# Optimization experiments

Hardware: AMD Instinct MI355X
Metric: run time of the kernel (lower is better)

The kernel has to match this reference:

```python
import jax, jax.numpy as jnp
import numpy as np

N, D_IN, H, M = 16384, 360, 512, 2048


def _linear(x, W, b):
    return x @ W.T + b


def _bidir_softmax(Q, K):
    # score[i, j] = <Q_i, K_j>
    s = Q @ K.T                      # [N, M]
    return jax.nn.softmax(s, axis=0), jax.nn.softmax(s, axis=1)


def _read(Q, K):
    sq, sm = _bidir_softmax(Q, K)
    upd = Q * (jax.lax.stop_gradient(sm) @ K)   # elementwise gate by attended memory
    return upd, sq, sm


def _un_read(Q, K):
    # scores computed against -K, but memory combine still uses K (as in torch source)
    sq, sm = _bidir_softmax(Q, -K)
    upd = Q * (jax.lax.stop_gradient(sm) @ K)
    return upd, sq, sm


def _upload(Q, K):
    sq, sm = _bidir_softmax(Q, K)
    m, d = K.shape
    g = jnp.argmax(sm, axis=1)                       # top-1 slot per query  [N]
    col_max = jnp.max(sq, axis=0)                    # max over queries per slot [m]
    n = Q.shape[0]
    w = sq[jnp.arange(n), g] / col_max[g]            # per-query weight [N]
    # vectorized form of the per-slot python loop: scatter-reduce weighted queries
    query_update = jax.ops.segment_sum(w[:, None] * Q, g, num_segments=m)  # [m, d]
    upd = query_update + K
    norm = jnp.linalg.norm(upd, axis=1, keepdims=True)
    upd = upd / jnp.maximum(norm, 1e-12)             # F.normalize(dim=1)
    return jax.lax.stop_gradient(upd)


def setup_inputs() -> dict:
    key = jax.random.key(0)
    ks = jax.random.split(key, 12)
    s = 0.02
    return {
        "x": jax.random.normal(ks[0], (N, D_IN), jnp.float32),
        "m_items_1": jax.random.normal(ks[1], (M, H), jnp.float32),
        "W1": jax.random.normal(ks[2], (H, D_IN), jnp.float32) * s,
        "b1": jnp.zeros((H,), jnp.float32),
        "W2": jax.random.normal(ks[3], (H, H), jnp.float32) * s,
        "b2": jnp.zeros((H,), jnp.float32),
        "W3": jax.random.normal(ks[4], (H, H), jnp.float32) * s,
        "b3": jnp.zeros((H,), jnp.float32),
        "Wd": jax.random.normal(ks[5], (1, H), jnp.float32) * s,
        "bd": jnp.zeros((1,), jnp.float32),
        "train": 1,
    }


def reference(x, m_items_1, W1, b1, W2, b2, W3, b3, Wd, bd, train):
    h = jax.nn.relu(_linear(x, W1, b1))
    h = jax.nn.relu(_linear(h, W2, b2))   # dropout=0.0 -> identity
    h = jax.nn.relu(_linear(h, W3, b3))
    pred_min_p, _, _ = _read(h, m_items_1)
    pred_min_n, _, _ = _un_read(h, m_items_1)
    mem = _upload(h, m_items_1) if train else m_items_1
    pred = _linear(h, Wd, bd)
    return (pred, pred_min_n, pred_min_p, mem)
```

## Files before the change

kernel.cpp:

```cpp
#include <hip/hip_runtime.h>
#include <math.h>

#define N_ROWS 16384
#define D_INN  360
#define KP1    384
#define HID    512
#define M_SLOTS 2048

typedef __attribute__((ext_vector_type(8))) short short8v;
typedef __attribute__((ext_vector_type(4))) float f32x4;
typedef __attribute__((address_space(1))) unsigned int as1_uint;
typedef __attribute__((address_space(3))) unsigned int as3_uint;

__device__ __forceinline__ unsigned short bf16_rne(float f){
  unsigned u = __float_as_uint(f);
  unsigned r = u + 0x7FFFu + ((u >> 16) & 1u);
  return (unsigned short)(r >> 16);
}
__device__ __forceinline__ float bf16_to_f32(unsigned short h){
  return __uint_as_float(((unsigned)h) << 16);
}

__device__ __forceinline__ unsigned fmap(float f){
  unsigned u = __float_as_uint(f);
  return (u & 0x80000000u) ? ~u : (u | 0x80000000u);
}
__device__ __forceinline__ float funmap(unsigned u){
  unsigned b = (u & 0x80000000u) ? (u ^ 0x80000000u) : ~u;
  return __uint_as_float(b);
}

__device__ __forceinline__ void glds16(const void* g, void* l){
  __builtin_amdgcn_global_load_lds((const as1_uint*)g, (as3_uint*)l, 16, 0, 0);
}

__device__ __forceinline__ float4 ld4bf(const unsigned short* hi, const unsigned short* lo, size_t off){
  uint2 h = *(const uint2*)(hi + off);
  uint2 l = *(const uint2*)(lo + off);
  float4 r;
  r.x = bf16_to_f32((unsigned short)(h.x & 0xffffu)) + bf16_to_f32((unsigned short)(l.x & 0xffffu));
  r.y = bf16_to_f32((unsigned short)(h.x >> 16))     + bf16_to_f32((unsigned short)(l.x >> 16));
  r.z = bf16_to_f32((unsigned short)(h.y & 0xffffu)) + bf16_to_f32((unsigned short)(l.y & 0xffffu));
  r.w = bf16_to_f32((unsigned short)(h.y >> 16))     + bf16_to_f32((unsigned short)(l.y >> 16));
  return r;
}


__device__ __forceinline__ void split_body(const float* __restrict__ src,
                                           unsigned short* __restrict__ hi,
                                           unsigned short* __restrict__ lo, int b){
  int idx = (b*256 + (int)threadIdx.x) * 8;
  float4 a = *(const float4*)&src[idx];
  float4 bb = *(const float4*)&src[idx+4];
  float v[8] = {a.x,a.y,a.z,a.w,bb.x,bb.y,bb.z,bb.w};
  short8v hv, lv;
#pragma unroll
  for (int e=0;e<8;++e){
    unsigned short h = bf16_rne(v[e]);
    hv[e] = (short)h;
    lv[e] = (short)bf16_rne(v[e] - bf16_to_f32(h));
  }
  *(short8v*)&hi[idx] = hv;
  *(short8v*)&lo[idx] = lv;
}

__device__ __forceinline__ void pad_split_body(const float* __restrict__ src,
                                               unsigned short* __restrict__ hi,
                                               unsigned short* __restrict__ lo,
                                               int R, int Ksrc, int Kp, int b){
  long long e0 = ((long long)b*256 + threadIdx.x) * 4;
  if (e0 >= (long long)R*Kp) return;
  int row = (int)(e0 / Kp), c = (int)(e0 % Kp);
  unsigned short h4[4], l4[4];
  if (c < Ksrc){
    float4 v = *(const float4*)&src[(size_t)row*Ksrc + c];
    float vv[4] = {v.x, v.y, v.z, v.w};
#pragma unroll
    for (int e=0;e<4;++e){
      unsigned short h = bf16_rne(vv[e]);
      h4[e] = h;
      l4[e] = bf16_rne(vv[e] - bf16_to_f32(h));
    }
  } else {
#pragma unroll
    for (int e=0;e<4;++e){ h4[e]=0; l4[e]=0; }
  }
  *(uint2*)&hi[(size_t)row*Kp + c] = *(uint2*)h4;
  *(uint2*)&lo[(size_t)row*Kp + c] = *(uint2*)l4;
}

__global__ __launch_bounds__(256) void init_all(
    const float* __restrict__ x,  const float* __restrict__ W1,
    const float* __restrict__ W2, const float* __restrict__ W3,
    const float* __restrict__ Km,
    unsigned short* __restrict__ xph,  unsigned short* __restrict__ xpl,
    unsigned short* __restrict__ W1ph, unsigned short* __restrict__ W1pl,
    unsigned short* __restrict__ W2h,  unsigned short* __restrict__ W2l,
    unsigned short* __restrict__ W3h,  unsigned short* __restrict__ W3l,
    unsigned short* __restrict__ Khi,  unsigned short* __restrict__ Klo,
    unsigned short* __restrict__ Kt,
    float* __restrict__ qacc, int* __restrict__ cnt,
    unsigned* __restrict__ colmaxU)
{
  __shared__ float tile[64][65];
  int b = blockIdx.x;
  const int t = threadIdx.x;
  if (b < 6144){ pad_split_body(x, xph, xpl, N_ROWS, D_INN, KP1, b); return; }
  b -= 6144;
  if (b < 192){ pad_split_body(W1, W1ph, W1pl, HID, D_INN, KP1, b); return; }
  b -= 192;
  if (b < 128){ split_body(W2, W2h, W2l, b); return; }
  b -= 128;
  if (b < 128){ split_body(W3, W3h, W3l, b); return; }
  b -= 128;
  if (b < 512){ split_body(Km, Khi, Klo, b); return; }
  b -= 512;
  if (b < 256){
    const int sb = (b & 31) * 64;
    const int hb = (b >> 5) * 64;
    {
      int r = t >> 2, cq = t & 3;
#pragma unroll
      for (int q=0;q<4;++q){
        float4 v = *(const float4*)&Km[(size_t)(sb+r)*HID + hb + cq*16 + q*4];
        tile[r][cq*16+q*4+0]=v.x; tile[r][cq*16+q*4+1]=v.y;
        tile[r][cq*16+q*4+2]=v.z; tile[r][cq*16+q*4+3]=v.w;
      }
    }
    __syncthreads();
    {
      int hl = t >> 2, sq = t & 3;
      unsigned short w16[16];
#pragma unroll
      for (int q=0;q<16;++q) w16[q] = bf16_rne(tile[sq*16+q][hl]);
      *(uint4*)&Kt[(size_t)(hb+hl)*M_SLOTS + sb + sq*16]     = *(uint4*)&w16[0];
      *(uint4*)&Kt[(size_t)(hb+hl)*M_SLOTS + sb + sq*16 + 8] = *(uint4*)&w16[8];
    }
    return;
  }
  b -= 256;
  if (b < 512){
    int idx = (b*256 + t)*8;
    float4 z = {0.f,0.f,0.f,0.f};
    *(float4*)&qacc[idx]     = z;
    *(float4*)&qacc[idx + 4] = z;
    return;
  }
  b -= 512;
  { int i = b*256 + t; if (i < M_SLOTS){ cnt[i] = 0; colmaxU[i] = 0u; } }
}

__global__ __launch_bounds__(512) void mlp_gemm(
    const unsigned short* __restrict__ Ah_g, const unsigned short* __restrict__ Al_g,
    const unsigned short* __restrict__ Wh_g, const unsigned short* __restrict__ Wl_g,
    const float* __restrict__ bias,
    unsigned short* __restrict__ Ohi, unsigned short* __restrict__ Olo,
    int Kp, const float* __restrict__ Wd, float* __restrict__ ppart)
{
  __shared__ char smem[65536];
  unsigned short* Ah = (unsigned short*)smem;
  unsigned short* Al = (unsigned short*)(smem + 16384);
  unsigned short* Bh = (unsigned short*)(smem + 32768);
  unsigned short* Bl = (unsigned short*)(smem + 49152);
  const int t = threadIdx.x;
  const int lane = t & 63, w = t >> 6;
  const int l15 = lane & 15, l4 = lane >> 4;
  const int rowBase = blockIdx.x * 128;
  const int colBase = blockIdx.y * 128;
  const int wr = (w >> 1) * 32;
  const int wc = (w & 1) * 64;

  f32x4 acc[2][4];
#pragma unroll
  for (int i=0;i<2;++i)
#pragma unroll
    for (int j=0;j<4;++j) acc[i][j] = (f32x4){0.f,0.f,0.f,0.f};

  const int nkt = Kp >> 6;
  for (int kt = 0; kt < nkt; ++kt){
    const int k0 = kt * 64;
#pragma unroll
    for (int p = 0; p < 2; ++p){
      int idx = p*512 + t;
      int r = idx >> 3, c = idx & 7;
      int cc = c ^ (r & 7);
      size_t go = (size_t)(rowBase + r) * Kp + (k0 + cc*8);
      glds16(Ah_g + go, (char*)Ah + idx*16);
      glds16(Al_g + go, (char*)Al + idx*16);
    }
#pragma unroll
    for (int p = 0; p < 2; ++p){
      int idx = p*512 + t;
      int r = idx >> 3, c = idx & 7;
      int cc = c ^ (r & 7);
      size_t go = (size_t)(colBase + r) * Kp + (k0 + cc*8);
      glds16(Wh_g + go, (char*)Bh + idx*16);
      glds16(Wl_g + go, (char*)Bl + idx*16);
    }
    __syncthreads();

#pragma unroll
    for (int s = 0; s < 2; ++s){
      short8v a_h[2], a_l[2], b_h[4], b_l[4];
#pragma unroll
      for (int rt = 0; rt < 2; ++rt){
        int r = wr + rt*16 + l15;
        int off = r*128 + ((s*4 + l4) ^ (r & 7))*16;
        a_h[rt] = *(const short8v*)((const char*)Ah + off);
        a_l[rt] = *(const short8v*)((const char*)Al + off);
      }
#pragma unroll
      for (int ct = 0; ct < 4; ++ct){
        int r = wc + ct*16 + l15;
        int off = r*128 + ((s*4 + l4) ^ (r & 7))*16;
        b_h[ct] = *(const short8v*)((const char*)Bh + off);
        b_l[ct] = *(const short8v*)((const char*)Bl + off);
      }
#pragma unroll
      for (int rt = 0; rt < 2; ++rt)
#pragma unroll
        for (int ct = 0; ct < 4; ++ct){
          acc[rt][ct] = __builtin_amdgcn_mfma_f32_16x16x32_bf16(a_h[rt], b_h[ct], acc[rt][ct], 0,0,0);
          acc[rt][ct] = __builtin_amdgcn_mfma_f32_16x16x32_bf16(a_h[rt], b_l[ct], acc[rt][ct], 0,0,0);
          acc[rt][ct] = __builtin_amdgcn_mfma_f32_16x16x32_bf16(a_l[rt], b_h[ct], acc[rt][ct], 0,0,0);
        }
    }
    __syncthreads();
  }

  float bcol[4];
#pragma unroll
  for (int ct=0; ct<4; ++ct) bcol[ct] = bias[colBase + wc + ct*16 + l15];
  unsigned short* Sout = (unsigned short*)smem;
#pragma unroll
  for (int rt=0; rt<2; ++rt)
#pragma unroll
    for (int ct=0; ct<4; ++ct)
#pragma unroll
      for (int reg=0; reg<4; ++reg){
        float v = acc[rt][ct][reg] + bcol[ct];
        v = v > 0.f ? v : 0.f;
        acc[rt][ct][reg] = v;
        Sout[(wr + rt*16 + l4*4 + reg)*136 + wc + ct*16 + l15] = bf16_rne(v);
      }

  if (ppart){
    float wdv[4];
#pragma unroll
    for (int ct=0; ct<4; ++ct) wdv[ct] = Wd[colBase + wc + ct*16 + l15];
#pragma unroll
    for (int rt=0; rt<2; ++rt)
#pragma unroll
      for (int reg=0; reg<4; ++reg){
        float pd = acc[rt][0][reg]*wdv[0] + acc[rt][1][reg]*wdv[1]
                 + acc[rt][2][reg]*wdv[2] + acc[rt][3][reg]*wdv[3];
#pragma unroll
        for (int d=1; d<16; d<<=1) pd += __shfl_xor(pd, d);
        if (l15 == 0){
          int row = rowBase + wr + rt*16 + l4*4 + reg;
          ppart[(size_t)row*8 + (colBase >> 7)*2 + (wc >> 6)] = pd;
        }
      }
  }

  __syncthreads();
#pragma unroll
  for (int p = 0; p < 4; ++p){
    int row = (t >> 4) + p*32;
    int c8 = (t & 15) * 8;
    uint4 v = *(uint4*)&Sout[row*136 + c8];
    *(uint4*)&Ohi[(size_t)(rowBase+row)*HID + colBase + c8] = v;
  }
  __syncthreads();
#pragma unroll
  for (int rt=0; rt<2; ++rt)
#pragma unroll
    for (int ct=0; ct<4; ++ct)
#pragma unroll
      for (int reg=0; reg<4; ++reg){
        float v = acc[rt][ct][reg];
        unsigned short h = bf16_rne(v);
        Sout[(wr + rt*16 + l4*4 + reg)*136 + wc + ct*16 + l15] = bf16_rne(v - bf16_to_f32(h));
      }
  __syncthreads();
#pragma unroll
  for (int p = 0; p < 4; ++p){
    int row = (t >> 4) + p*32;
    int c8 = (t & 15) * 8;
    uint4 v = *(uint4*)&Sout[row*136 + c8];
    *(uint4*)&Olo[(size_t)(rowBase+row)*HID + colBase + c8] = v;
  }
}

__global__ __launch_bounds__(512) void sgemm_stats(
    const unsigned short* __restrict__ Qhi, const unsigned short* __restrict__ Qlo,
    const unsigned short* __restrict__ Khi, const unsigned short* __restrict__ Klo,
    unsigned short* __restrict__ Sb,
    float* __restrict__ pmax, int* __restrict__ pcol,
    float* __restrict__ psum, float* __restrict__ pnmax, float* __restrict__ pnsum,
    unsigned* __restrict__ colmaxU)
{
  __shared__ char smem[65536];
  unsigned short* Ah = (unsigned short*)smem;
  unsigned short* Al = (unsigned short*)(smem + 16384);
  unsigned short* Bh = (unsigned short*)(smem + 32768);
  unsigned short* Bl = (unsigned short*)(smem + 49152);
  const int t = threadIdx.x;
  const int lane = t & 63, w = t >> 6;
  const int l15 = lane & 15, l4 = lane >> 4;
  const int cb = blockIdx.x;
  const int rb = blockIdx.y;
  const int rowBase = rb * 128;
  const int colBase = cb * 128;
  const int wr = (w >> 1) * 32;
  const int wc = (w & 1) * 64;

  f32x4 acc[2][4];
#pragma unroll
  for (int i=0;i<2;++i)
#pragma unroll
    for (int j=0;j<4;++j) acc[i][j] = (f32x4){0.f,0.f,0.f,0.f};

  for (int kt = 0; kt < 8; ++kt){
    const int k0 = kt * 64;
#pragma unroll
    for (int p = 0; p < 2; ++p){
      int idx = p*512 + t;
      int r = idx >> 3, c = idx & 7;
      int cc = c ^ (r & 7);
      size_t go = (size_t)(rowBase + r) * HID + (k0 + cc*8);
      glds16(Qhi + go, (char*)Ah + idx*16);
      glds16(Qlo + go, (char*)Al + idx*16);
    }
#pragma unroll
    for (int p = 0; p < 2; ++p){
      int idx = p*512 + t;
      int r = idx >> 3, c = idx & 7;
      int cc = c ^ (r & 7);
      size_t go = (size_t)(colBase + r) * HID + (k0 + cc*8);
      glds16(Khi + go, (char*)Bh + idx*16);
      glds16(Klo + go, (char*)Bl + idx*16);
    }
    __syncthreads();

#pragma unroll
    for (int s = 0; s < 2; ++s){
      short8v a_h[2], a_l[2], b_h[4], b_l[4];
#pragma unroll
      for (int rt = 0; rt < 2; ++rt){
        int r = wr + rt*16 + l15;
        int off = r*128 + ((s*4 + l4) ^ (r & 7))*16;
        a_h[rt] = *(const short8v*)((const char*)Ah + off);
        a_l[rt] = *(const short8v*)((const char*)Al + off);
      }
#pragma unroll
      for (int ct = 0; ct < 4; ++ct){
        int r = wc + ct*16 + l15;
        int off = r*128 + ((s*4 + l4) ^ (r & 7))*16;
        b_h[ct] = *(const short8v*)((const char*)Bh + off);
        b_l[ct] = *(const short8v*)((const char*)Bl + off);
      }
#pragma unroll
      for (int rt = 0; rt < 2; ++rt)
#pragma unroll
        for (int ct = 0; ct < 4; ++ct){
          acc[rt][ct] = __builtin_amdgcn_mfma_f32_16x16x32_bf16(a_h[rt], b_h[ct], acc[rt][ct], 0,0,0);
          acc[rt][ct] = __builtin_amdgcn_mfma_f32_16x16x32_bf16(a_h[rt], b_l[ct], acc[rt][ct], 0,0,0);
          acc[rt][ct] = __builtin_amdgcn_mfma_f32_16x16x32_bf16(a_l[rt], b_h[ct], acc[rt][ct], 0,0,0);
        }
    }
    __syncthreads();
  }

#pragma unroll
  for (int rt = 0; rt < 2; ++rt){
#pragma unroll
    for (int reg = 0; reg < 4; ++reg){
      float v0 = acc[rt][0][reg], v1 = acc[rt][1][reg];
      float v2 = acc[rt][2][reg], v3 = acc[rt][3][reg];
      float bvv = v0; int bcc = colBase + wc + l15;
      if (v1 > bvv){ bvv = v1; bcc = colBase + wc + 16 + l15; }
      if (v2 > bvv){ bvv = v2; bcc = colBase + wc + 32 + l15; }
      if (v3 > bvv){ bvv = v3; bcc = colBase + wc + 48 + l15; }
      float mnv = fminf(fminf(v0,v1), fminf(v2,v3));
#pragma unroll
      for (int d = 1; d < 16; d <<= 1){
        float ov = __shfl_xor(bvv, d);
        int   oc = __shfl_xor(bcc, d);
        float om = __shfl_xor(mnv, d);
        if (ov > bvv || (ov == bvv && oc < bcc)){ bvv = ov; bcc = oc; }
        mnv = fminf(mnv, om);
      }
      float sp = __expf(v0-bvv)+__expf(v1-bvv)+__expf(v2-bvv)+__expf(v3-bvv);
      float sn = __expf(mnv-v0)+__expf(mnv-v1)+__expf(mnv-v2)+__expf(mnv-v3);
#pragma unroll
      for (int d = 1; d < 16; d <<= 1){ sp += __shfl_xor(sp,d); sn += __shfl_xor(sn,d); }
      if (l15 == 0){
        int row = rowBase + wr + rt*16 + l4*4 + reg;
        size_t pi = (size_t)row*32 + cb*2 + (w & 1);
        pmax[pi] = bvv; pcol[pi] = bcc; psum[pi] = sp;
        pnmax[pi] = -mnv; pnsum[pi] = sn;
      }
    }
  }

#pragma unroll
  for (int ct = 0; ct < 4; ++ct){
    float cm = -1e30f;
#pragma unroll
    for (int rt=0; rt<2; ++rt)
#pragma unroll
      for (int reg=0; reg<4; ++reg) cm = fmaxf(cm, acc[rt][ct][reg]);
    cm = fmaxf(cm, __shfl_xor(cm, 16));
    cm = fmaxf(cm, __shfl_xor(cm, 32));
    if (l4 == 0)
      atomicMax(&colmaxU[colBase + wc + ct*16 + l15], fmap(cm));
  }

  __syncthreads();
  unsigned short* Sout = (unsigned short*)smem;
#pragma unroll
  for (int rt=0; rt<2; ++rt)
#pragma unroll
    for (int ct=0; ct<4; ++ct)
#pragma unroll
      for (int reg=0; reg<4; ++reg)
        Sout[(wr + rt*16 + l4*4 + reg)*136 + wc + ct*16 + l15] = bf16_rne(acc[rt][ct][reg]);
  __syncthreads();
#pragma unroll
  for (int p = 0; p < 4; ++p){
    int row = (t >> 4) + p*32;
    int c8 = (t & 15) * 8;
    uint4 v = *(uint4*)&Sout[row*136 + c8];
    *(uint4*)&Sb[(size_t)(rowBase+row)*M_SLOTS + colBase + c8] = v;
  }
}

__global__ __launch_bounds__(256) void merge_all(
    const float* __restrict__ pmax, const int* __restrict__ pcol,
    const float* __restrict__ psum, const float* __restrict__ pnmax,
    const float* __restrict__ pnsum,
    float* __restrict__ rowm, float* __restrict__ rsp,
    float* __restrict__ rmn, float* __restrict__ rsn, int* __restrict__ gidx,
    int* __restrict__ cnt,
    const float* __restrict__ ppart, const float* __restrict__ bd,
    float* __restrict__ pred)
{
  int row = blockIdx.x*256 + threadIdx.x;
  const size_t base = (size_t)row*32;
  float m = -1e30f; int g = 0;
  for (int i=0;i<32;++i){
    float v = pmax[base+i];
    if (v > m){ m = v; g = pcol[base+i]; }
  }
  float s = 0.f;
  for (int i=0;i<32;++i) s += psum[base+i] * __expf(pmax[base+i]-m);
  float mn = -1e30f;
  for (int i=0;i<32;++i) mn = fmaxf(mn, pnmax[base+i]);
  float sn = 0.f;
  for (int i=0;i<32;++i) sn += pnsum[base+i] * __expf(pnmax[base+i]-mn);
  rowm[row]=m; gidx[row]=g; rsp[row]=1.f/s; rmn[row]=mn; rsn[row]=1.f/sn;
  atomicAdd(&cnt[g], 1);
  float pd = bd[0];
#pragma unroll
  for (int i=0;i<8;++i) pd += ppart[(size_t)row*8 + i];
  pred[row] = pd;
}

#define PV_RB 64
#define PV_HB 256
__global__ __launch_bounds__(512) void pv2(
    const unsigned short* __restrict__ Sb, const unsigned short* __restrict__ Kt,
    const float* __restrict__ rowm, const float* __restrict__ rsp,
    const float* __restrict__ rmn, const float* __restrict__ rsn,
    const unsigned short* __restrict__ Qhi, const unsigned short* __restrict__ Qlo,
    float* __restrict__ outP, float* __restrict__ outN)
{
  __shared__ char smem[49152];
  unsigned short* Ktile = (unsigned short*)smem;
  unsigned short* Wp = (unsigned short*)(smem + 32768);
  unsigned short* Wn = (unsigned short*)(smem + 40960);
  const int t = threadIdx.x, lane = t & 63, w = t >> 6;
  const int l15 = lane & 15, l4 = lane >> 4;
  const int rowBase = blockIdx.y * PV_RB;
  const int hBase = blockIdx.x * PV_HB;
  const int wrq = (w >> 2) * 32;
  const int hw = (w & 3) * 64;
  const int rS = t >> 3;
  const int c8 = t & 7;
  const float mp = rowm[rowBase + rS], mn = rmn[rowBase + rS];

  f32x4 accP[2][4], accN[2][4];
#pragma unroll
  for (int i=0;i<2;++i)
#pragma unroll
    for (int j=0;j<4;++j){ accP[i][j]=(f32x4){0.f,0.f,0.f,0.f}; accN[i][j]=(f32x4){0.f,0.f,0.f,0.f}; }

  for (int kt = 0; kt < 32; ++kt){
    const int k0 = kt*64;
#pragma unroll
    for (int p=0;p<4;++p){
      int idx = p*512 + t;
      int r = idx >> 3, c = idx & 7;
      int cc = c ^ (r & 7);
      glds16(Kt + (size_t)(hBase + r)*M_SLOTS + k0 + cc*8, (char*)Ktile + idx*16);
    }
    short8v sv = *(const short8v*)&Sb[(size_t)(rowBase + rS)*M_SLOTS + k0 + c8*8];
    short8v wp, wn;
#pragma unroll
    for (int e=0;e<8;++e){
      float sval = bf16_to_f32((unsigned short)sv[e]);
      wp[e] = (short)bf16_rne(__expf(sval - mp));
      wn[e] = (short)bf16_rne(__expf(-sval - mn));
    }
    {
      int ch = rS*8 + (c8 ^ (rS & 7));
      *(short8v*)(Wp + ch*8) = wp;
      *(short8v*)(Wn + ch*8) = wn;
    }
    __syncthreads();
#pragma unroll
    for (int s=0; s<2; ++s){
      short8v ap[2], an[2], b[4];
#pragma unroll
      for (int rt=0; rt<2; ++rt){
        int r = wrq + rt*16 + l15;
        int ch = r*8 + ((s*4 + l4) ^ (r & 7));
        ap[rt] = *(const short8v*)(Wp + ch*8);
        an[rt] = *(const short8v*)(Wn + ch*8);
      }
#pragma unroll
      for (int ct=0; ct<4; ++ct){
        int hr = hw + ct*16 + l15;
        b[ct] = *(const short8v*)((const char*)Ktile + hr*128 + ((s*4 + l4) ^ (hr & 7))*16);
      }
#pragma unroll
      for (int rt=0; rt<2; ++rt)
#pragma unroll
        for (int ct=0; ct<4; ++ct){
          accP[rt][ct] = __builtin_amdgcn_mfma_f32_16x16x32_bf16(ap[rt], b[ct], accP[rt][ct], 0,0,0);
          accN[rt][ct] = __builtin_amdgcn_mfma_f32_16x16x32_bf16(an[rt], b[ct], accN[rt][ct], 0,0,0);
        }
    }
    __syncthreads();
  }

  float isp[2][4], isn[2][4];
#pragma unroll
  for (int rt=0; rt<2; ++rt)
#pragma unroll
    for (int reg=0; reg<4; ++reg){
      int row = rowBase + wrq + rt*16 + l4*4 + reg;
      isp[rt][reg] = rsp[row];
      isn[rt][reg] = rsn[row];
    }
  float* Pout = (float*)smem;
#pragma unroll
  for (int sign=0; sign<2; ++sign){
#pragma unroll
    for (int rh=0; rh<2; ++rh){
      if ((w >> 2) == rh){
#pragma unroll
        for (int rt=0; rt<2; ++rt)
#pragma unroll
          for (int ct=0; ct<4; ++ct)
#pragma unroll
            for (int reg=0; reg<4; ++reg){
              float v = sign ? accN[rt][ct][reg]*isn[rt][reg]
                             : accP[rt][ct][reg]*isp[rt][reg];
              Pout[(rt*16 + l4*4 + reg)*260 + hw + ct*16 + l15] = v;
            }
      }
      __syncthreads();
      float* outX = sign ? outN : outP;
#pragma unroll
      for (int p=0; p<4; ++p){
        int row = t >> 4;
        int col = (t & 15)*4 + p*64;
        int grow = rowBase + rh*32 + row;
        float4 pv = *(float4*)&Pout[row*260 + col];
        float4 qv = ld4bf(Qhi, Qlo, (size_t)grow*HID + hBase + col);
        float4 o; o.x=pv.x*qv.x; o.y=pv.y*qv.y; o.z=pv.z*qv.z; o.w=pv.w*qv.w;
        *(float4*)&outX[(size_t)grow*HID + hBase + col] = o;
      }
      __syncthreads();
    }
  }
}


__global__ __launch_bounds__(256) void csr_scan(const int* __restrict__ cnt,
                                                int* __restrict__ off, int* __restrict__ woff){
  __shared__ int partial[256];
  const int t = threadIdx.x;
  const int base = t*8;
  int local[8]; int s = 0;
#pragma unroll
  for (int j=0;j<8;++j){ local[j] = s; s += cnt[base+j]; }
  partial[t] = s;
  __syncthreads();
  for (int d=1; d<256; d<<=1){
    int v = (t>=d) ? partial[t-d] : 0;
    __syncthreads();
    partial[t] += v;
    __syncthreads();
  }
  int pre = (t==0) ? 0 : partial[t-1];
#pragma unroll
  for (int j=0;j<8;++j){ int o = pre + local[j]; off[base+j]=o; woff[base+j]=o; }
  if (t==255) off[2048] = partial[255];
}

__global__ __launch_bounds__(256) void csr_fill(const int* __restrict__ gidx,
                                                const float* __restrict__ rowm,
                                                const unsigned* __restrict__ colmaxU,
                                                int* __restrict__ woff,
                                                int* __restrict__ rows, float* __restrict__ wv,
                                                int* __restrict__ sid){
  int i = blockIdx.x*256 + threadIdx.x;
  int g = gidx[i];
  int p = atomicAdd(&woff[g], 1);
  rows[p] = i;
  wv[p] = __expf(rowm[i] - funmap(colmaxU[g]));
  sid[p] = g;
}

__global__ __launch_bounds__(256) void upload_scatter(
    const unsigned short* __restrict__ Qhi, const unsigned short* __restrict__ Qlo,
    const int* __restrict__ sid, const int* __restrict__ rows, const float* __restrict__ wv,
    const int* __restrict__ train, float* __restrict__ qacc)
{
  if (*train == 0) return;
  const int b = blockIdx.x, t = threadIdx.x;
  __shared__ int   s_sid[64];
  __shared__ int   s_row[64];
  __shared__ float s_w[64];
  if (t < 64){
    int p = b*64 + t;
    s_sid[t] = sid[p];
    s_row[t] = rows[p];
    s_w[t]   = wv[p];
  }
  __syncthreads();
  const int h0 = t*2;
  float a0 = 0.f, a1 = 0.f;
  int prev = s_sid[0];
#pragma unroll 4
  for (int p = 0; p < 64; ++p){
    int s = s_sid[p];
    if (s != prev){
      atomicAdd(&qacc[(size_t)prev*HID + h0],     a0);
      atomicAdd(&qacc[(size_t)prev*HID + h0 + 1], a1);
      a0 = 0.f; a1 = 0.f; prev = s;
    }
    int row = s_row[p];
    float w = s_w[p];
    unsigned h = *(const unsigned*)(Qhi + (size_t)row*HID + h0);
    unsigned l = *(const unsigned*)(Qlo + (size_t)row*HID + h0);
    a0 += w * (bf16_to_f32((unsigned short)(h & 0xffffu)) + bf16_to_f32((unsigned short)(l & 0xffffu)));
    a1 += w * (bf16_to_f32((unsigned short)(h >> 16))     + bf16_to_f32((unsigned short)(l >> 16)));
  }
  atomicAdd(&qacc[(size_t)prev*HID + h0],     a0);
  atomicAdd(&qacc[(size_t)prev*HID + h0 + 1], a1);
}

__global__ __launch_bounds__(256) void upload_finish(const float* __restrict__ qacc,
                                                     const float* __restrict__ Km,
                                                     const int* __restrict__ train,
                                                     float* __restrict__ mem)
{
  const int m = blockIdx.x, t = threadIdx.x;
  const int h0 = t * 2;
  float2 kv = *(const float2*)&Km[(size_t)m*HID + h0];
  if (*train == 0){
    mem[(size_t)m*HID + h0]     = kv.x;
    mem[(size_t)m*HID + h0 + 1] = kv.y;
    return;
  }
  float2 av = *(const float2*)&qacc[(size_t)m*HID + h0];
  float v0 = av.x + kv.x, v1 = av.y + kv.y;
  __shared__ float red[256];
  red[t] = v0*v0 + v1*v1;
  __syncthreads();
  for (int s = 128; s > 0; s >>= 1){
    if (t < s) red[t] += red[t + s];
    __syncthreads();
  }
  float rinv = 1.f / fmaxf(sqrtf(red[0]), 1e-12f);
  mem[(size_t)m*HID + h0]     = v0 * rinv;
  mem[(size_t)m*HID + h0 + 1] = v1 * rinv;
}


extern "C" void kernel_launch(void* const* d_in, const int* in_sizes, int n_in,
                              void* d_out, int out_size, void* d_ws, size_t ws_size,
                              hipStream_t stream)
{
  const float* x   = (const float*)d_in[0];
  const float* Km  = (const float*)d_in[1];
  const float* W1  = (const float*)d_in[2];
  const float* b1  = (const float*)d_in[3];
  const float* W2  = (const float*)d_in[4];
  const float* b2  = (const float*)d_in[5];
  const float* W3  = (const float*)d_in[6];
  const float* b3  = (const float*)d_in[7];
  const float* Wd  = (const float*)d_in[8];
  const float* bd  = (const float*)d_in[9];
  const int* train = (const int*)d_in[10];

  float* out  = (float*)d_out;
  float* pred = out;
  float* outN = out + 16384;
  float* outP = out + 16384 + 8388608;
  float* memo = out + 16384 + 2*8388608;

  char* ws = (char*)d_ws;
  unsigned short* Qhi   = (unsigned short*)(ws + 0);
  unsigned short* Qlo   = (unsigned short*)(ws + 16777216);
  unsigned short* xph   = (unsigned short*)(ws + 33554432);
  unsigned short* xpl   = (unsigned short*)(ws + 46137344);
  unsigned short* h1h   = (unsigned short*)(ws + 58720256);
  unsigned short* h1l   = (unsigned short*)(ws + 75497472);
  unsigned short* h2h   = (unsigned short*)(ws + 92274688);
  unsigned short* h2l   = (unsigned short*)(ws + 109051904);
  unsigned short* Sb    = (unsigned short*)(ws + 33554432);
  unsigned short* Khi   = (unsigned short*)(ws + 125829120);
  unsigned short* Klo   = (unsigned short*)(ws + 127926272);
  unsigned short* Kt    = (unsigned short*)(ws + 130023424);
  unsigned short* W1ph  = (unsigned short*)(ws + 132120576);
  unsigned short* W1pl  = (unsigned short*)(ws + 132513792);
  unsigned short* W2h   = (unsigned short*)(ws + 132907008);
  unsigned short* W2l   = (unsigned short*)(ws + 133431296);
  unsigned short* W3h   = (unsigned short*)(ws + 133955584);
  unsigned short* W3l   = (unsigned short*)(ws + 134479872);
  float* pmax    = (float*)(ws + 135004160);
  int*   pcol    = (int*)  (ws + 137101312);
  float* psum    = (float*)(ws + 139198464);
  float* pnmax   = (float*)(ws + 141295616);
  float* pnsum   = (float*)(ws + 143392768);
  float* rowm    = (float*)(ws + 149684224);
  float* rsp     = (float*)(ws + 149749760);
  float* rmn     = (float*)(ws + 149815296);
  float* rsn     = (float*)(ws + 149880832);
  int*   gidx    = (int*)  (ws + 149946368);
  unsigned* colmaxU = (unsigned*)(ws + 150011904);
  int*   cnt     = (int*)  (ws + 150020096);
  int*   off     = (int*)  (ws + 150028288);
  int*   woff    = (int*)  (ws + 150036736);
  int*   rows    = (int*)  (ws + 150044928);
  float* wv      = (float*)(ws + 150110464);
  int*   sid     = (int*)  (ws + 150176000);
  float* qacc    = (float*)(ws + 150241536);
  float* ppart   = (float*)(ws + 154435840);
  const size_t NEED = 154960128ull;
  if (ws_size < NEED) return;

  dim3 blk(256);

  init_all<<<7880, blk, 0, stream>>>(x, W1, W2, W3, Km,
                                     xph, xpl, W1ph, W1pl, W2h, W2l, W3h, W3l,
                                     Khi, Klo, Kt, qacc, cnt, colmaxU);

  mlp_gemm<<<dim3(N_ROWS/128, 4), dim3(512), 0, stream>>>(xph, xpl, W1ph, W1pl, b1, h1h, h1l, KP1,
                                                          (const float*)nullptr, (float*)nullptr);
  mlp_gemm<<<dim3(N_ROWS/128, 4), dim3(512), 0, stream>>>(h1h, h1l, W2h, W2l, b2, h2h, h2l, HID,
                                                          (const float*)nullptr, (float*)nullptr);
  mlp_gemm<<<dim3(N_ROWS/128, 4), dim3(512), 0, stream>>>(h2h, h2l, W3h, W3l, b3, Qhi, Qlo, HID,
                                                          Wd, ppart);

  sgemm_stats<<<dim3(16, 128), dim3(512), 0, stream>>>(Qhi, Qlo, Khi, Klo, Sb,
                                                       pmax, pcol, psum, pnmax, pnsum, colmaxU);
  merge_all<<<64, blk, 0, stream>>>(pmax, pcol, psum, pnmax, pnsum,
                                    rowm, rsp, rmn, rsn, gidx, cnt, ppart, bd, pred);
  pv2<<<dim3(2, 256), dim3(512), 0, stream>>>(Sb, Kt, rowm, rsp, rmn, rsn, Qhi, Qlo, outP, outN);

  csr_scan<<<1, blk, 0, stream>>>(cnt, off, woff);
  csr_fill<<<N_ROWS/256, blk, 0, stream>>>(gidx, rowm, colmaxU, woff, rows, wv, sid);
  upload_scatter<<<N_ROWS/64, blk, 0, stream>>>(Qhi, Qlo, sid, rows, wv, train, qacc);
  upload_finish<<<M_SLOTS, blk, 0, stream>>>(qacc, Km, train, memo);
}
```

Baseline: 396.4 us.

## Swizzle block order in score and PV GEMMs, fold CSR scan into fill

Measured after the change: 386.4 us. 1.03x faster.

```diff
diff --git a/kernel.cpp b/kernel.cpp
--- a/kernel.cpp
+++ b/kernel.cpp
@@ -100,7 +100,7 @@
     unsigned short* __restrict__ Khi,  unsigned short* __restrict__ Klo,
     unsigned short* __restrict__ Kt,
     float* __restrict__ qacc, int* __restrict__ cnt,
-    unsigned* __restrict__ colmaxU)
+    unsigned* __restrict__ colmaxU, int* __restrict__ woff)
 {
   __shared__ float tile[64][65];
   int b = blockIdx.x;
@@ -147,7 +147,7 @@
     return;
   }
   b -= 512;
-  { int i = b*256 + t; if (i < M_SLOTS){ cnt[i] = 0; colmaxU[i] = 0u; } }
+  { int i = b*256 + t; if (i < M_SLOTS){ cnt[i] = 0; colmaxU[i] = 0u; woff[i] = 0; } }
 }
 
 __global__ __launch_bounds__(512) void mlp_gemm(
@@ -308,8 +308,10 @@
   const int t = threadIdx.x;
   const int lane = t & 63, w = t >> 6;
   const int l15 = lane & 15, l4 = lane >> 4;
-  const int cb = blockIdx.x;
-  const int rb = blockIdx.y;
+  const int flat = blockIdx.x + 16*blockIdx.y;
+  const int swz  = (flat & 7)*256 + (flat >> 3);
+  const int cb = swz & 15;
+  const int rb = swz >> 4;
   const int rowBase = rb * 128;
   const int colBase = cb * 128;
   const int wr = (w >> 1) * 32;
@@ -482,8 +484,10 @@
   unsigned short* Wn = (unsigned short*)(smem + 40960);
   const int t = threadIdx.x, lane = t & 63, w = t >> 6;
   const int l15 = lane & 15, l4 = lane >> 4;
-  const int rowBase = blockIdx.y * PV_RB;
-  const int hBase = blockIdx.x * PV_HB;
+  const int flat = blockIdx.x + 2*blockIdx.y;
+  const int swz  = (flat & 7)*64 + (flat >> 3);
+  const int rowBase = (swz >> 1) * PV_RB;
+  const int hBase = (swz & 1) * PV_HB;
   const int wrq = (w >> 2) * 32;
   const int hw = (w & 3) * 64;
   const int rS = t >> 3;
@@ -588,38 +592,35 @@
   }
 }
 
-
-__global__ __launch_bounds__(256) void csr_scan(const int* __restrict__ cnt,
-                                                int* __restrict__ off, int* __restrict__ woff){
-  __shared__ int partial[256];
-  const int t = threadIdx.x;
-  const int base = t*8;
-  int local[8]; int s = 0;
-#pragma unroll
-  for (int j=0;j<8;++j){ local[j] = s; s += cnt[base+j]; }
-  partial[t] = s;
-  __syncthreads();
-  for (int d=1; d<256; d<<=1){
-    int v = (t>=d) ? partial[t-d] : 0;
-    __syncthreads();
-    partial[t] += v;
-    __syncthreads();
-  }
-  int pre = (t==0) ? 0 : partial[t-1];
-#pragma unroll
-  for (int j=0;j<8;++j){ int o = pre + local[j]; off[base+j]=o; woff[base+j]=o; }
-  if (t==255) off[2048] = partial[255];
-}
-
-__global__ __launch_bounds__(256) void csr_fill(const int* __restrict__ gidx,
+__global__ __launch_bounds__(256) void csr_fill(const int* __restrict__ cnt,
+                                                const int* __restrict__ gidx,
                                                 const float* __restrict__ rowm,
                                                 const unsigned* __restrict__ colmaxU,
                                                 int* __restrict__ woff,
                                                 int* __restrict__ rows, float* __restrict__ wv,
                                                 int* __restrict__ sid){
-  int i = blockIdx.x*256 + threadIdx.x;
+  __shared__ int s_off[M_SLOTS];
+  __shared__ int partial[256];
+  const int t = threadIdx.x;
+  const int base = t*8;
+  int local[8]; int s = 0;
+#pragma unroll
+  for (int j=0;j<8;++j){ local[j] = s; s += cnt[base+j]; }
+  partial[t] = s;
+  __syncthreads();
+  for (int d=1; d<256; d<<=1){
+    int v = (t>=d) ? partial[t-d] : 0;
+    __syncthreads();
+    partial[t] += v;
+    __syncthreads();
+  }
+  int pre = (t==0) ? 0 : partial[t-1];
+#pragma unroll
+  for (int j=0;j<8;++j) s_off[base+j] = pre + local[j];
+  __syncthreads();
+  int i = blockIdx.x*256 + t;
   int g = gidx[i];
-  int p = atomicAdd(&woff[g], 1);
+  int p = s_off[g] + atomicAdd(&woff[g], 1);
   rows[p] = i;
   wv[p] = __expf(rowm[i] - funmap(colmaxU[g]));
   sid[p] = g;
@@ -745,7 +746,6 @@
   int*   gidx    = (int*)  (ws + 149946368);
   unsigned* colmaxU = (unsigned*)(ws + 150011904);
   int*   cnt     = (int*)  (ws + 150020096);
-  int*   off     = (int*)  (ws + 150028288);
   int*   woff    = (int*)  (ws + 150036736);
   int*   rows    = (int*)  (ws + 150044928);
   float* wv      = (float*)(ws + 150110464);
@@ -759,7 +759,7 @@
 
   init_all<<<7880, blk, 0, stream>>>(x, W1, W2, W3, Km,
                                      xph, xpl, W1ph, W1pl, W2h, W2l, W3h, W3l,
-                                     Khi, Klo, Kt, qacc, cnt, colmaxU);
+                                     Khi, Klo, Kt, qacc, cnt, colmaxU, woff);
 
   mlp_gemm<<<dim3(N_ROWS/128, 4), dim3(512), 0, stream>>>(xph, xpl, W1ph, W1pl, b1, h1h, h1l, KP1,
                                                           (const float*)nullptr, (float*)nullptr);
@@ -774,8 +774,7 @@
                                     rowm, rsp, rmn, rsn, gidx, cnt, ppart, bd, pred);
   pv2<<<dim3(2, 256), dim3(512), 0, stream>>>(Sb, Kt, rowm, rsp, rmn, rsn, Qhi, Qlo, outP, outN);
 
-  csr_scan<<<1, blk, 0, stream>>>(cnt, off, woff);
-  csr_fill<<<N_ROWS/256, blk, 0, stream>>>(gidx, rowm, colmaxU, woff, rows, wv, sid);
+  csr_fill<<<N_ROWS/256, blk, 0, stream>>>(cnt, gidx, rowm, colmaxU, woff, rows, wv, sid);
   upload_scatter<<<N_ROWS/64, blk, 0, stream>>>(Qhi, Qlo, sid, rows, wv, train, qacc);
   upload_finish<<<M_SLOTS, blk, 0, stream>>>(qacc, Km, train, memo);
 }
```
